# Kernel optimization log

Measured on AMD Instinct MI355X. Metric: run time of the kernel, lower is better.

The kernel has to match this reference:

```python
import jax, jax.numpy as jnp
import numpy as np

E = 1024
H = 16
D = E // H  # head_dim = 64
B, S = 8, 1024


def setup_inputs() -> dict:
    key = jax.random.key(0)
    ks = jax.random.split(key, 5)
    x = jax.random.normal(ks[0], (B, S, E), dtype=jnp.float32)
    # nn.Linear(E, 3E): weight [3E, E], bias [3E]
    w_in = jax.random.normal(ks[1], (3 * E, E), dtype=jnp.float32) * (1.0 / np.sqrt(E))
    b_in = jax.random.normal(ks[2], (3 * E,), dtype=jnp.float32) * 0.02
    # nn.Linear(E, E)
    w_out = jax.random.normal(ks[3], (E, E), dtype=jnp.float32) * (1.0 / np.sqrt(E))
    b_out = jax.random.normal(ks[4], (E,), dtype=jnp.float32) * 0.02
    return {"x": x, "w_in": w_in, "b_in": b_in, "w_out": w_out, "b_out": b_out}


def reference(x, w_in, b_in, w_out, b_out):
    Bb, Ss, _ = x.shape
    # fused QKV projection: x @ W.T + b -> [B, S, 3E]
    qkv = jnp.einsum('bse,fe->bsf', x, w_in) + b_in
    # reshape to [B, H, S, 3D] then split
    qkv = qkv.reshape(Bb, Ss, H, 3 * D).transpose(0, 2, 1, 3)
    q, k, v = jnp.split(qkv, 3, axis=-1)  # each [B, H, S, D]
    scale = 1.0 / jnp.sqrt(jnp.asarray(D, dtype=x.dtype))
    logits = jnp.einsum('bhqd,bhkd->bhqk', q, k) * scale  # [B, H, S, S]
    attn = jax.nn.softmax(logits, axis=-1)
    values = jnp.einsum('bhqk,bhkd->bhqd', attn, v)  # [B, H, S, D]
    values = values.transpose(0, 2, 1, 3).reshape(Bb, Ss, E)
    out = jnp.einsum('bse,fe->bsf', values, w_out) + b_out
    return out
```

## Files before the change

### kernel.cpp

```cpp
#include <hip/hip_runtime.h>

typedef short short8 __attribute__((ext_vector_type(8)));
typedef float f32x4 __attribute__((ext_vector_type(4)));

#define AS1 __attribute__((address_space(1)))
#define AS3 __attribute__((address_space(3)))

__device__ __forceinline__ void gload16(const void* g, void* l) {
    __builtin_amdgcn_global_load_lds((const AS1 unsigned int*)g, (AS3 unsigned int*)l, 16, 0, 0);
}

__device__ __forceinline__ unsigned short f2bf(float f) {
    union { float f; unsigned u; } c; c.f = f;
    unsigned r = (c.u + 0x7FFFu + ((c.u >> 16) & 1u)) >> 16;
    return (unsigned short)r;
}

__device__ __forceinline__ unsigned cvtpk(float a, float b) {
    unsigned r;
    asm("v_cvt_pk_bf16_f32 %0, %1, %2" : "=v"(r) : "v"(a), "v"(b));
    return r;
}

__device__ __forceinline__ void mfma16(f32x4& d, short8 a, short8 b) {
    asm("v_mfma_f32_16x16x32_bf16 %0, %1, %2, %0" : "+v"(d) : "v"(a), "v"(b));
}

#define QSCALE 0.18033688011112042f
#define SMREF 24.0f

#define XN4 2097152
#define WIN4 786432
#define WOUT4 262144
__global__ __launch_bounds__(256) void cvt_all(const float* __restrict__ x,
                                               const float* __restrict__ w_in,
                                               const float* __restrict__ w_out,
                                               unsigned short* __restrict__ xb,
                                               unsigned short* __restrict__ winb,
                                               unsigned short* __restrict__ woutb) {
    int idx = blockIdx.x * 256 + threadIdx.x;
    int stride = gridDim.x * 256;
    for (int i = idx; i < XN4 + WIN4 + WOUT4; i += stride) {
        const float4* src;
        ushort4* dst;
        int j;
        if (i < XN4) {
            src = (const float4*)x; dst = (ushort4*)xb; j = i;
        } else if (i < XN4 + WIN4) {
            src = (const float4*)w_in; dst = (ushort4*)winb; j = i - XN4;
        } else {
            src = (const float4*)w_out; dst = (ushort4*)woutb; j = i - XN4 - WIN4;
        }
        float4 v = src[j];
        ushort4 o;
        o.x = f2bf(v.x); o.y = f2bf(v.y); o.z = f2bf(v.z); o.w = f2bf(v.w);
        dst[j] = o;
    }
}

__global__ __launch_bounds__(256, 2) void gemm_qkv(
    const unsigned short* __restrict__ A, const unsigned short* __restrict__ B,
    const float* __restrict__ bias, int K,
    unsigned short* __restrict__ qb, unsigned short* __restrict__ kb,
    unsigned short* __restrict__ vtb) {
    __shared__ unsigned short As[256 * 64];
    __shared__ unsigned short Bs[128 * 64];
    const int tid = threadIdx.x;
    const int lane = tid & 63;
    const int wv = tid >> 6;
    const int lr = lane & 15, lg = lane >> 4;
    const int x7 = lr & 7;
    const int m0 = blockIdx.x * 256, n0 = blockIdx.y * 128;

    f32x4 acc[4][8];
#pragma unroll
    for (int i = 0; i < 4; i++)
#pragma unroll
        for (int j = 0; j < 8; j++) acc[i][j] = (f32x4){0.f, 0.f, 0.f, 0.f};

    const int sr = tid >> 3;
    const int sc = ((tid & 7) ^ ((tid >> 3) & 7)) * 8;
    const unsigned short* Ag = A + (size_t)(m0 + sr) * K + sc;
    const unsigned short* Bg = B + (size_t)(n0 + sr) * K + sc;
    unsigned short* Asl = As + tid * 8;
    unsigned short* Bsl = Bs + tid * 8;

    for (int kt = 0; kt < K; kt += 64) {
        __syncthreads();
#pragma unroll
        for (int i = 0; i < 8; i++)
            gload16(Ag + (size_t)(i * 32) * K + kt, Asl + i * 2048);
#pragma unroll
        for (int i = 0; i < 4; i++)
            gload16(Bg + (size_t)(i * 32) * K + kt, Bsl + i * 2048);
        __syncthreads();
#pragma unroll
        for (int ks = 0; ks < 2; ks++) {
            const int co = ((ks * 4 + lg) ^ x7) * 8;
            short8 af[4], bf[8];
#pragma unroll
            for (int mi = 0; mi < 4; mi++)
                af[mi] = *(const short8*)(As + (wv * 64 + mi * 16 + lr) * 64 + co);
#pragma unroll
            for (int ni = 0; ni < 8; ni++)
                bf[ni] = *(const short8*)(Bs + (ni * 16 + lr) * 64 + co);
            __builtin_amdgcn_s_setprio(1);
#pragma unroll
            for (int mi = 0; mi < 4; mi++)
#pragma unroll
                for (int ni = 0; ni < 8; ni++) mfma16(acc[mi][ni], af[mi], bf[ni]);
            __builtin_amdgcn_s_setprio(0);
        }
    }

#pragma unroll
    for (int ni = 0; ni < 8; ni++) {
        const int col = n0 + ni * 16 + lr;
        const float bia = bias[col];
        const unsigned h = (unsigned)col / 192u;
        const int rem = col - (int)h * 192;
        const int tq = rem >> 6, d = rem & 63;
#pragma unroll
        for (int mi = 0; mi < 4; mi++) {
            const int row = m0 + wv * 64 + mi * 16 + lg * 4;
            const int bb = row >> 10, s = row & 1023;
            const int bh = bb * 16 + (int)h;
            if (tq == 0) {
#pragma unroll
                for (int r = 0; r < 4; r++)
                    qb[((size_t)bh * 1024 + s + r) * 64 + d] =
                        f2bf((acc[mi][ni][r] + bia) * QSCALE);
            } else if (tq == 1) {
#pragma unroll
                for (int r = 0; r < 4; r++)
                    kb[((size_t)bh * 1024 + s + r) * 64 + d] = f2bf(acc[mi][ni][r] + bia);
            } else {
                uint2 pk;
                pk.x = cvtpk(acc[mi][ni][0] + bia, acc[mi][ni][1] + bia);
                pk.y = cvtpk(acc[mi][ni][2] + bia, acc[mi][ni][3] + bia);
                *(uint2*)(vtb + ((size_t)bh * 64 + d) * 1024 + s) = pk;
            }
        }
    }
}

__global__ __launch_bounds__(256) void gemm_proj(
    const unsigned short* __restrict__ A, const unsigned short* __restrict__ B,
    const float* __restrict__ bias, int K, int N, float* __restrict__ Cf) {
    __shared__ unsigned short As[128 * 64];
    __shared__ unsigned short Bs[128 * 64];
    const int tid = threadIdx.x;
    const int lane = tid & 63;
    const int wv = tid >> 6;
    const int wm = (wv >> 1) * 64, wn = (wv & 1) * 64;
    const int lr = lane & 15, lg = lane >> 4;
    const int x7 = lr & 7;
    const int m0 = blockIdx.x * 128, n0 = blockIdx.y * 128;

    f32x4 acc[4][4];
#pragma unroll
    for (int i = 0; i < 4; i++)
#pragma unroll
        for (int j = 0; j < 4; j++) acc[i][j] = (f32x4){0.f, 0.f, 0.f, 0.f};

    const int sr = tid >> 3;
    const int sc = ((tid & 7) ^ ((tid >> 3) & 7)) * 8;
    const unsigned short* Ag = A + (size_t)(m0 + sr) * K + sc;
    const unsigned short* Bg = B + (size_t)(n0 + sr) * K + sc;
    unsigned short* Asl = As + tid * 8;
    unsigned short* Bsl = Bs + tid * 8;

    for (int kt = 0; kt < K; kt += 64) {
        __syncthreads();
#pragma unroll
        for (int i = 0; i < 4; i++) {
            gload16(Ag + (size_t)(i * 32) * K + kt, Asl + i * 2048);
            gload16(Bg + (size_t)(i * 32) * K + kt, Bsl + i * 2048);
        }
        __syncthreads();
#pragma unroll
        for (int ks = 0; ks < 2; ks++) {
            short8 af[4], bf[4];
#pragma unroll
            for (int mi = 0; mi < 4; mi++)
                af[mi] = *(const short8*)(As + (wm + mi * 16 + lr) * 64 +
                                          (((ks * 4 + lg) ^ x7) * 8));
#pragma unroll
            for (int ni = 0; ni < 4; ni++)
                bf[ni] = *(const short8*)(Bs + (wn + ni * 16 + lr) * 64 +
                                          (((ks * 4 + lg) ^ x7) * 8));
            __builtin_amdgcn_s_setprio(1);
#pragma unroll
            for (int mi = 0; mi < 4; mi++)
#pragma unroll
                for (int ni = 0; ni < 4; ni++) mfma16(acc[mi][ni], af[mi], bf[ni]);
            __builtin_amdgcn_s_setprio(0);
        }
    }

#pragma unroll
    for (int ni = 0; ni < 4; ni++) {
        const int col = n0 + wn + ni * 16 + lr;
        const float bia = bias[col];
#pragma unroll
        for (int mi = 0; mi < 4; mi++) {
            const int row = m0 + wm + mi * 16 + lg * 4;
#pragma unroll
            for (int r = 0; r < 4; r++)
                Cf[(size_t)(row + r) * N + col] = acc[mi][ni][r] + bia;
        }
    }
}

__device__ __forceinline__ void softmax_half(f32x4 (&s)[4], float& lpart,
                                             unsigned short* pbuf,
                                             int lr, int lg, int x7) {
    float p[4][4];
#pragma unroll
    for (int kt = 0; kt < 4; kt++)
#pragma unroll
        for (int r = 0; r < 4; r++) {
            p[kt][r] = __builtin_amdgcn_exp2f(s[kt][r] - SMREF);
            lpart += p[kt][r];
        }
#pragma unroll
    for (int kt = 0; kt < 4; kt++)
#pragma unroll
        for (int w2 = 0; w2 < 2; w2++) {
            const unsigned pk = cvtpk(p[kt][2 * w2], p[kt][2 * w2 + 1]);
            const int col = (kt * 16 + lg * 4 + 2 * w2) ^ (x7 << 3);
            *(unsigned*)(pbuf + lr * 64 + col) = pk;
        }
}

__global__ __launch_bounds__(256) void attn_fwd(
    const unsigned short* __restrict__ qg, const unsigned short* __restrict__ kg,
    const unsigned short* __restrict__ vtg, unsigned short* __restrict__ vals) {
    __shared__ unsigned short Ks[2][64 * 64];
    __shared__ unsigned short Vts[2][64 * 64];
    __shared__ unsigned short Ps[4 * 2048];
    const int tid = threadIdx.x, lane = tid & 63, w = tid >> 6;
    const int lr = lane & 15, lg = lane >> 4;
    const int x7 = lr & 7;
    const int bh = blockIdx.x;
    const int q0 = blockIdx.y * 128 + w * 32;

    const unsigned short* qrowA = qg + ((size_t)bh * 1024 + q0 + lr) * 64;
    const unsigned short* qrowB = qrowA + 16 * 64;
    short8 qA[2], qB[2];
    qA[0] = *(const short8*)(qrowA + lg * 8);
    qA[1] = *(const short8*)(qrowA + 32 + lg * 8);
    qB[0] = *(const short8*)(qrowB + lg * 8);
    qB[1] = *(const short8*)(qrowB + 32 + lg * 8);

    f32x4 oA[4], oB[4];
    float lA = 0.f, lB = 0.f;
#pragma unroll
    for (int i = 0; i < 4; i++) {
        oA[i] = (f32x4){0.f, 0.f, 0.f, 0.f};
        oB[i] = (f32x4){0.f, 0.f, 0.f, 0.f};
    }

    const unsigned short* kb = kg + (size_t)bh * 65536;
    const unsigned short* vb = vtg + (size_t)bh * 65536;
    unsigned short* pwl = Ps + w * 2048;

    const int srow = tid >> 3;
    const int scol = ((tid & 7) ^ (srow & 7)) * 8;

    auto stage = [&](int kv0, int buf) {
#pragma unroll
        for (int i = 0; i < 2; i++) {
            gload16(kb + (size_t)(kv0 + i * 32 + srow) * 64 + scol,
                    &Ks[buf][i * 2048 + tid * 8]);
            gload16(vb + (size_t)(i * 32 + srow) * 1024 + kv0 + scol,
                    &Vts[buf][i * 2048 + tid * 8]);
        }
    };

    stage(0, 0);
    __syncthreads();

    for (int t = 0; t < 16; ++t) {
        const int buf = t & 1;
        if (t < 15) stage((t + 1) * 64, buf ^ 1);
        const unsigned short* Kb = Ks[buf];
        const unsigned short* Vb = Vts[buf];

        f32x4 sA[4], sB[4];
#pragma unroll
        for (int i = 0; i < 4; i++) {
            sA[i] = (f32x4){0.f, 0.f, 0.f, 0.f};
            sB[i] = (f32x4){0.f, 0.f, 0.f, 0.f};
        }
#pragma unroll
        for (int kt = 0; kt < 4; kt++) {
            const short8 k0 = *(const short8*)(Kb + (kt * 16 + lr) * 64 + ((0 + lg) ^ x7) * 8);
            const short8 k1 = *(const short8*)(Kb + (kt * 16 + lr) * 64 + ((4 + lg) ^ x7) * 8);
            __builtin_amdgcn_s_setprio(1);
            mfma16(sA[kt], k0, qA[0]);
            mfma16(sB[kt], k0, qB[0]);
            mfma16(sA[kt], k1, qA[1]);
            mfma16(sB[kt], k1, qB[1]);
            __builtin_amdgcn_s_setprio(0);
        }

        softmax_half(sA, lA, pwl, lr, lg, x7);
        softmax_half(sB, lB, pwl + 1024, lr, lg, x7);

        short8 pA[2], pB[2];
#pragma unroll
        for (int ks2 = 0; ks2 < 2; ks2++) {
            pA[ks2] = *(const short8*)(pwl + lr * 64 + (((ks2 * 4 + lg) ^ x7) * 8));
            pB[ks2] = *(const short8*)(pwl + 1024 + lr * 64 + (((ks2 * 4 + lg) ^ x7) * 8));
        }
#pragma unroll
        for (int mi = 0; mi < 4; mi++) {
            const short8 v0 = *(const short8*)(Vb + (mi * 16 + lr) * 64 + ((0 + lg) ^ x7) * 8);
            const short8 v1 = *(const short8*)(Vb + (mi * 16 + lr) * 64 + ((4 + lg) ^ x7) * 8);
            __builtin_amdgcn_s_setprio(1);
            mfma16(oA[mi], v0, pA[0]);
            mfma16(oB[mi], v0, pB[0]);
            mfma16(oA[mi], v1, pA[1]);
            mfma16(oB[mi], v1, pB[1]);
            __builtin_amdgcn_s_setprio(0);
        }

        __syncthreads();
    }

    lA += __shfl_xor(lA, 16); lA += __shfl_xor(lA, 32);
    lB += __shfl_xor(lB, 16); lB += __shfl_xor(lB, 32);

    const int bb = bh >> 4, hh = bh & 15;
    {
        const float inv = 1.f / lA;
        unsigned short* vp = vals + (size_t)(bb * 1024 + q0 + lr) * 1024 + hh * 64 + lg * 4;
#pragma unroll
        for (int mi = 0; mi < 4; mi++) {
            uint2 st;
            st.x = cvtpk(oA[mi][0] * inv, oA[mi][1] * inv);
            st.y = cvtpk(oA[mi][2] * inv, oA[mi][3] * inv);
            *(uint2*)(vp + mi * 16) = st;
        }
    }
    {
        const float inv = 1.f / lB;
        unsigned short* vp = vals + (size_t)(bb * 1024 + q0 + 16 + lr) * 1024 + hh * 64 + lg * 4;
#pragma unroll
        for (int mi = 0; mi < 4; mi++) {
            uint2 st;
            st.x = cvtpk(oB[mi][0] * inv, oB[mi][1] * inv);
            st.y = cvtpk(oB[mi][2] * inv, oB[mi][3] * inv);
            *(uint2*)(vp + mi * 16) = st;
        }
    }
}

extern "C" void kernel_launch(void* const* d_in, const int* in_sizes, int n_in,
                              void* d_out, int out_size, void* d_ws, size_t ws_size,
                              hipStream_t stream) {
    const float* x = (const float*)d_in[0];
    const float* w_in = (const float*)d_in[1];
    const float* b_in = (const float*)d_in[2];
    const float* w_out = (const float*)d_in[3];
    const float* b_out = (const float*)d_in[4];
    float* out = (float*)d_out;

    unsigned short* ws = (unsigned short*)d_ws;
    unsigned short* xb = ws;
    unsigned short* winb = xb + 8388608;
    unsigned short* woutb = winb + 3145728;
    unsigned short* qb = woutb + 1048576;
    unsigned short* kb = qb + 8388608;
    unsigned short* vtb = kb + 8388608;
    unsigned short* vals = xb;

    cvt_all<<<2048, 256, 0, stream>>>(x, w_in, w_out, xb, winb, woutb);

    gemm_qkv<<<dim3(32, 24), 256, 0, stream>>>(xb, winb, b_in, 1024, qb, kb, vtb);
    attn_fwd<<<dim3(128, 8), 256, 0, stream>>>(qb, kb, vtb, vals);
    gemm_proj<<<dim3(64, 8), 256, 0, stream>>>(vals, woutb, b_out, 1024, 1024, out);
}
```

Before: 157.7 us.

## Double-buffer QKV GEMM with smaller 128x128 tiles and 2x2 wave layout

Rewrites the QKV projection GEMM to use 128x128 block tiles with a K-step of 32. The LDS buffers are double-buffered so the next tile's global-to-LDS loads are issued before the current tile's MFMAs, and each K-step needs only one barrier instead of two. Waves are arranged 2x2 with 64x64 sub-tiles, and the grid doubles to 64x24 blocks. This shrinks the accumulator footprint and removes the occupancy hint, trading per-block operand reuse and arithmetic intensity for overlap of loads with compute and more resident blocks.

```diff
diff --git a/kernel.cpp b/kernel.cpp
--- a/kernel.cpp
+++ b/kernel.cpp
@@ -58,71 +58,74 @@
     }
 }
 
-__global__ __launch_bounds__(256, 2) void gemm_qkv(
+__global__ __launch_bounds__(256) void gemm_qkv(
     const unsigned short* __restrict__ A, const unsigned short* __restrict__ B,
     const float* __restrict__ bias, int K,
     unsigned short* __restrict__ qb, unsigned short* __restrict__ kb,
     unsigned short* __restrict__ vtb) {
-    __shared__ unsigned short As[256 * 64];
-    __shared__ unsigned short Bs[128 * 64];
+    __shared__ unsigned short As[2][128 * 32];
+    __shared__ unsigned short Bs[2][128 * 32];
     const int tid = threadIdx.x;
     const int lane = tid & 63;
     const int wv = tid >> 6;
+    const int wm = (wv >> 1) * 64, wn = (wv & 1) * 64;
     const int lr = lane & 15, lg = lane >> 4;
-    const int x7 = lr & 7;
-    const int m0 = blockIdx.x * 256, n0 = blockIdx.y * 128;
-
-    f32x4 acc[4][8];
+    const int xr = (lr >> 1) & 3;
+    const int m0 = blockIdx.x * 128, n0 = blockIdx.y * 128;
+
+    f32x4 acc[4][4];
 #pragma unroll
     for (int i = 0; i < 4; i++)
 #pragma unroll
-        for (int j = 0; j < 8; j++) acc[i][j] = (f32x4){0.f, 0.f, 0.f, 0.f};
-
-    const int sr = tid >> 3;
-    const int sc = ((tid & 7) ^ ((tid >> 3) & 7)) * 8;
-    const unsigned short* Ag = A + (size_t)(m0 + sr) * K + sc;
-    const unsigned short* Bg = B + (size_t)(n0 + sr) * K + sc;
-    unsigned short* Asl = As + tid * 8;
-    unsigned short* Bsl = Bs + tid * 8;
-
-    for (int kt = 0; kt < K; kt += 64) {
+        for (int j = 0; j < 4; j++) acc[i][j] = (f32x4){0.f, 0.f, 0.f, 0.f};
+
+    const int srow = tid >> 2;
+    const int sgx = ((tid & 3) ^ ((tid >> 3) & 3)) * 8;
+    const unsigned short* Ag = A + (size_t)(m0 + srow) * K + sgx;
+    const unsigned short* Bg = B + (size_t)(n0 + srow) * K + sgx;
+
+    auto stage = [&](int kt, int buf) {
+#pragma unroll
+        for (int j = 0; j < 2; j++) {
+            gload16(Ag + (size_t)(j * 64) * K + kt, &As[buf][j * 2048 + tid * 8]);
+            gload16(Bg + (size_t)(j * 64) * K + kt, &Bs[buf][j * 2048 + tid * 8]);
+        }
+    };
+
+    stage(0, 0);
+    __syncthreads();
+
+    const int co = (lg ^ xr) * 8;
+    const int NT = K >> 5;
+    for (int t = 0; t < NT; ++t) {
+        const int buf = t & 1;
+        if (t + 1 < NT) stage((t + 1) << 5, buf ^ 1);
+        short8 af[4], bf[4];
+#pragma unroll
+        for (int mi = 0; mi < 4; mi++)
+            af[mi] = *(const short8*)(&As[buf][(wm + mi * 16 + lr) * 32 + co]);
+#pragma unroll
+        for (int ni = 0; ni < 4; ni++)
+            bf[ni] = *(const short8*)(&Bs[buf][(wn + ni * 16 + lr) * 32 + co]);
+        __builtin_amdgcn_s_setprio(1);
+#pragma unroll
+        for (int mi = 0; mi < 4; mi++)
+#pragma unroll
+            for (int ni = 0; ni < 4; ni++) mfma16(acc[mi][ni], af[mi], bf[ni]);
+        __builtin_amdgcn_s_setprio(0);
         __syncthreads();
-#pragma unroll
-        for (int i = 0; i < 8; i++)
-            gload16(Ag + (size_t)(i * 32) * K + kt, Asl + i * 2048);
-#pragma unroll
-        for (int i = 0; i < 4; i++)
-            gload16(Bg + (size_t)(i * 32) * K + kt, Bsl + i * 2048);
-        __syncthreads();
-#pragma unroll
-        for (int ks = 0; ks < 2; ks++) {
-            const int co = ((ks * 4 + lg) ^ x7) * 8;
-            short8 af[4], bf[8];
-#pragma unroll
-            for (int mi = 0; mi < 4; mi++)
-                af[mi] = *(const short8*)(As + (wv * 64 + mi * 16 + lr) * 64 + co);
-#pragma unroll
-            for (int ni = 0; ni < 8; ni++)
-                bf[ni] = *(const short8*)(Bs + (ni * 16 + lr) * 64 + co);
-            __builtin_amdgcn_s_setprio(1);
-#pragma unroll
-            for (int mi = 0; mi < 4; mi++)
-#pragma unroll
-                for (int ni = 0; ni < 8; ni++) mfma16(acc[mi][ni], af[mi], bf[ni]);
-            __builtin_amdgcn_s_setprio(0);
-        }
-    }
-
-#pragma unroll
-    for (int ni = 0; ni < 8; ni++) {
-        const int col = n0 + ni * 16 + lr;
+    }
+
+#pragma unroll
+    for (int ni = 0; ni < 4; ni++) {
+        const int col = n0 + wn + ni * 16 + lr;
         const float bia = bias[col];
         const unsigned h = (unsigned)col / 192u;
         const int rem = col - (int)h * 192;
         const int tq = rem >> 6, d = rem & 63;
 #pragma unroll
         for (int mi = 0; mi < 4; mi++) {
-            const int row = m0 + wv * 64 + mi * 16 + lg * 4;
+            const int row = m0 + wm + mi * 16 + lg * 4;
             const int bb = row >> 10, s = row & 1023;
             const int bh = bb * 16 + (int)h;
             if (tq == 0) {
@@ -378,7 +381,7 @@
 
     cvt_all<<<2048, 256, 0, stream>>>(x, w_in, w_out, xb, winb, woutb);
 
-    gemm_qkv<<<dim3(32, 24), 256, 0, stream>>>(xb, winb, b_in, 1024, qb, kb, vtb);
+    gemm_qkv<<<dim3(64, 24), 256, 0, stream>>>(xb, winb, b_in, 1024, qb, kb, vtb);
     attn_fwd<<<dim3(128, 8), 256, 0, stream>>>(qb, kb, vtb, vals);
     gemm_proj<<<dim3(64, 8), 256, 0, stream>>>(vals, woutb, b_out, 1024, 1024, out);
 }
```

Result: slower. 161.4 us (+2.3%).

## Widen QKV GEMM and attention blocks to 512 threads, drop setprio

Applied to the files above, without the earlier changes.

The QKV GEMM moves from 256 threads with a 256x128 tile (each wave computing 64x128) to 512 threads with a 128x256 tile, using a 2x4 wave grid where each wave computes 64x64. This lowers per-thread accumulator registers and spreads global-to-LDS staging over more threads. The attention kernel now uses 8 waves per block covering 256 query rows, so each K/V tile staged in LDS is shared by twice as many waves, and each thread issues half as many staging loads. The s_setprio hints around the MFMA loops are removed in both GEMMs. The trade-off is larger blocks, which may reduce the number of resident blocks and the scheduling flexibility.

```diff
diff --git a/kernel.cpp b/kernel.cpp
--- a/kernel.cpp
+++ b/kernel.cpp
@@ -58,71 +58,69 @@
     }
 }
 
-__global__ __launch_bounds__(256, 2) void gemm_qkv(
+__global__ __launch_bounds__(512) void gemm_qkv(
     const unsigned short* __restrict__ A, const unsigned short* __restrict__ B,
     const float* __restrict__ bias, int K,
     unsigned short* __restrict__ qb, unsigned short* __restrict__ kb,
     unsigned short* __restrict__ vtb) {
-    __shared__ unsigned short As[256 * 64];
-    __shared__ unsigned short Bs[128 * 64];
+    __shared__ unsigned short As[128 * 64];
+    __shared__ unsigned short Bs[256 * 64];
     const int tid = threadIdx.x;
     const int lane = tid & 63;
     const int wv = tid >> 6;
+    const int wm = (wv >> 2) * 64;
+    const int wn = (wv & 3) * 64;
     const int lr = lane & 15, lg = lane >> 4;
     const int x7 = lr & 7;
-    const int m0 = blockIdx.x * 256, n0 = blockIdx.y * 128;
-
-    f32x4 acc[4][8];
+    const int m0 = blockIdx.x * 128, n0 = blockIdx.y * 256;
+
+    f32x4 acc[4][4];
 #pragma unroll
     for (int i = 0; i < 4; i++)
 #pragma unroll
-        for (int j = 0; j < 8; j++) acc[i][j] = (f32x4){0.f, 0.f, 0.f, 0.f};
+        for (int j = 0; j < 4; j++) acc[i][j] = (f32x4){0.f, 0.f, 0.f, 0.f};
 
     const int sr = tid >> 3;
     const int sc = ((tid & 7) ^ ((tid >> 3) & 7)) * 8;
     const unsigned short* Ag = A + (size_t)(m0 + sr) * K + sc;
     const unsigned short* Bg = B + (size_t)(n0 + sr) * K + sc;
-    unsigned short* Asl = As + tid * 8;
-    unsigned short* Bsl = Bs + tid * 8;
 
     for (int kt = 0; kt < K; kt += 64) {
         __syncthreads();
 #pragma unroll
-        for (int i = 0; i < 8; i++)
-            gload16(Ag + (size_t)(i * 32) * K + kt, Asl + i * 2048);
-#pragma unroll
-        for (int i = 0; i < 4; i++)
-            gload16(Bg + (size_t)(i * 32) * K + kt, Bsl + i * 2048);
+        for (int j = 0; j < 2; j++)
+            gload16(Ag + (size_t)(j * 64) * K + kt, As + j * 4096 + tid * 8);
+#pragma unroll
+        for (int j = 0; j < 4; j++)
+            gload16(Bg + (size_t)(j * 64) * K + kt, Bs + j * 4096 + tid * 8);
         __syncthreads();
 #pragma unroll
         for (int ks = 0; ks < 2; ks++) {
             const int co = ((ks * 4 + lg) ^ x7) * 8;
-            short8 af[4], bf[8];
+            short8 af[4], bf[4];
 #pragma unroll
             for (int mi = 0; mi < 4; mi++)
-                af[mi] = *(const short8*)(As + (wv * 64 + mi * 16 + lr) * 64 + co);
-#pragma unroll
-            for (int ni = 0; ni < 8; ni++)
-                bf[ni] = *(const short8*)(Bs + (ni * 16 + lr) * 64 + co);
-            __builtin_amdgcn_s_setprio(1);
+                af[mi] = *(const short8*)(As + (wm + mi * 16 + lr) * 64 + co);
+#pragma unroll
+            for (int ni = 0; ni < 4; ni++)
+                bf[ni] = *(const short8*)(Bs + (wn + ni * 16 + lr) * 64 + co);
 #pragma unroll
             for (int mi = 0; mi < 4; mi++)
 #pragma unroll
-                for (int ni = 0; ni < 8; ni++) mfma16(acc[mi][ni], af[mi], bf[ni]);
-            __builtin_amdgcn_s_setprio(0);
-        }
-    }
-
-#pragma unroll
-    for (int ni = 0; ni < 8; ni++) {
-        const int col = n0 + ni * 16 + lr;
+                for (int ni = 0; ni < 4; ni++) mfma16(acc[mi][ni], af[mi], bf[ni]);
+        }
+    }
+
+#pragma unroll
+    for (int ni = 0; ni < 4; ni++) {
+        const int col = n0 + wn + ni * 16 + lr;
         const float bia = bias[col];
         const unsigned h = (unsigned)col / 192u;
         const int rem = col - (int)h * 192;
         const int tq = rem >> 6, d = rem & 63;
 #pragma unroll
         for (int mi = 0; mi < 4; mi++) {
-            const int row = m0 + wv * 64 + mi * 16 + lg * 4;
+            const int row = m0 + wm + mi * 16 + lg * 4;
             const int bb = row >> 10, s = row & 1023;
             const int bh = bb * 16 + (int)h;
             if (tq == 0) {
@@ -189,12 +187,10 @@
             for (int ni = 0; ni < 4; ni++)
                 bf[ni] = *(const short8*)(Bs + (wn + ni * 16 + lr) * 64 +
                                           (((ks * 4 + lg) ^ x7) * 8));
-            __builtin_amdgcn_s_setprio(1);
 #pragma unroll
             for (int mi = 0; mi < 4; mi++)
 #pragma unroll
                 for (int ni = 0; ni < 4; ni++) mfma16(acc[mi][ni], af[mi], bf[ni]);
-            __builtin_amdgcn_s_setprio(0);
         }
     }
 
@@ -233,17 +229,17 @@
         }
 }
 
-__global__ __launch_bounds__(256) void attn_fwd(
+__global__ __launch_bounds__(512) void attn_fwd(
     const unsigned short* __restrict__ qg, const unsigned short* __restrict__ kg,
     const unsigned short* __restrict__ vtg, unsigned short* __restrict__ vals) {
     __shared__ unsigned short Ks[2][64 * 64];
     __shared__ unsigned short Vts[2][64 * 64];
-    __shared__ unsigned short Ps[4 * 2048];
+    __shared__ unsigned short Ps[8 * 2048];
     const int tid = threadIdx.x, lane = tid & 63, w = tid >> 6;
     const int lr = lane & 15, lg = lane >> 4;
     const int x7 = lr & 7;
     const int bh = blockIdx.x;
-    const int q0 = blockIdx.y * 128 + w * 32;
+    const int q0 = blockIdx.y * 256 + w * 32;
 
     const unsigned short* qrowA = qg + ((size_t)bh * 1024 + q0 + lr) * 64;
     const unsigned short* qrowB = qrowA + 16 * 64;
@@ -269,13 +265,8 @@
     const int scol = ((tid & 7) ^ (srow & 7)) * 8;
 
     auto stage = [&](int kv0, int buf) {
-#pragma unroll
-        for (int i = 0; i < 2; i++) {
-            gload16(kb + (size_t)(kv0 + i * 32 + srow) * 64 + scol,
-                    &Ks[buf][i * 2048 + tid * 8]);
-            gload16(vb + (size_t)(i * 32 + srow) * 1024 + kv0 + scol,
-                    &Vts[buf][i * 2048 + tid * 8]);
-        }
+        gload16(kb + (size_t)(kv0 + srow) * 64 + scol, &Ks[buf][tid * 8]);
+        gload16(vb + (size_t)srow * 1024 + kv0 + scol, &Vts[buf][tid * 8]);
     };
 
     stage(0, 0);
@@ -378,7 +369,7 @@
 
     cvt_all<<<2048, 256, 0, stream>>>(x, w_in, w_out, xb, winb, woutb);
 
-    gemm_qkv<<<dim3(32, 24), 256, 0, stream>>>(xb, winb, b_in, 1024, qb, kb, vtb);
-    attn_fwd<<<dim3(128, 8), 256, 0, stream>>>(qb, kb, vtb, vals);
+    gemm_qkv<<<dim3(64, 12), 512, 0, stream>>>(xb, winb, b_in, 1024, qb, kb, vtb);
+    attn_fwd<<<dim3(128, 4), 512, 0, stream>>>(qb, kb, vtb, vals);
     gemm_proj<<<dim3(64, 8), 256, 0, stream>>>(vals, woutb, b_out, 1024, 1024, out);
 }
```

Result: faster. 145.7 us (-7.6%).
